# Kernel tuning notes

Measured on AMD Instinct MI355X. Metric: run time of the kernel, lower is better.

The kernel has to match this reference:

```python
import jax, jax.numpy as jnp
import numpy as np

S = 512            # sample_points along each ray
VD = VH = VW = 128  # voxel volume shape (drr.density.shape)
DET = 128           # detector H = W


def setup_inputs() -> dict:
    key = jax.random.key(0)
    k1, k2, k3 = jax.random.split(key, 3)
    B = 2
    pred_frontal = jax.random.uniform(k1, (B, 1, DET, DET), dtype=jnp.float32)
    pred_lateral = jax.random.uniform(k2, (B, 1, DET, DET), dtype=jnp.float32)
    ii, jj = jnp.meshgrid(jnp.arange(DET, dtype=jnp.float32),
                          jnp.arange(DET, dtype=jnp.float32), indexing='ij')
    # frontal: source behind volume on -z, detector plane at z=328
    source_F = jnp.array([[64.0, 64.0, -200.0]], dtype=jnp.float32)
    target_F = jnp.stack([ii, jj, jnp.full_like(ii, 328.0)], axis=-1)[None]  # (1,H,W,3)
    # lateral: source on -x, detector plane at x=328
    source_L = jnp.array([[-200.0, 64.0, 64.0]], dtype=jnp.float32)
    target_L = jnp.stack([jnp.full_like(ii, 328.0), ii, jj], axis=-1)[None]
    vol_gt_3d = jax.random.uniform(k3, (VD, VH, VW), dtype=jnp.float32)
    A_inv = jnp.eye(3, dtype=jnp.float32)   # drr.affine_inverse linear part
    t_inv = jnp.zeros(3, dtype=jnp.float32)  # drr.affine_inverse translation
    return {"pred_frontal": pred_frontal, "pred_lateral": pred_lateral,
            "source_F": source_F, "target_F": target_F,
            "source_L": source_L, "target_L": target_L,
            "vol_gt_3d": vol_gt_3d, "A_inv": A_inv, "t_inv": t_inv}


def _backproject(mask_2d, src, target_grid, A_inv, t_inv, threshold=0.5):
    # mask_2d: (H,W); src: (3,); target_grid: (H,W,3)
    active = (mask_2d > threshold).reshape(-1)          # (P,) bool
    det_pixels = target_grid.reshape(-1, 3)             # (P,3)
    ray_dirs = det_pixels - src[None, :]                 # (P,3)
    ray_len = jnp.linalg.norm(ray_dirs, axis=1, keepdims=True)  # (P,1)
    ray_dirs = ray_dirs / (ray_len + 1e-8)
    t_vals = jnp.linspace(0.0, 1.0, S, dtype=mask_2d.dtype)[None, :, None]  # (1,S,1)
    t_samples = t_vals * (ray_len[:, None, :] * 2.5)     # (P,S,1)
    world_pts = src[None, None, :] + ray_dirs[:, None, :] * t_samples  # (P,S,3)
    voxel = jnp.round(world_pts @ A_inv.T + t_inv).astype(jnp.int32)   # (P,S,3)
    valid = (active[:, None]
             & (voxel[..., 0] >= 0) & (voxel[..., 0] < VD)
             & (voxel[..., 1] >= 0) & (voxel[..., 1] < VH)
             & (voxel[..., 2] >= 0) & (voxel[..., 2] < VW))
    vi = jnp.clip(voxel, 0, jnp.array([VD - 1, VH - 1, VW - 1], dtype=jnp.int32))
    vol = jnp.zeros((VD, VH, VW), dtype=mask_2d.dtype)
    # set-to-1 scatter: max with {0,1} values; invalid samples write 0 (no-op)
    vol = vol.at[vi[..., 0], vi[..., 1], vi[..., 2]].max(valid.astype(mask_2d.dtype))
    return vol


def reference(pred_frontal, pred_lateral, source_F, target_F,
              source_L, target_L, vol_gt_3d, A_inv, t_inv):
    src_F, tgt_F = source_F[0], target_F[0]
    src_L, tgt_L = source_L[0], target_L[0]
    B = pred_frontal.shape[0]
    total = jnp.zeros((), dtype=pred_frontal.dtype)
    for i in range(B):
        vol_F = _backproject(pred_frontal[i, 0], src_F, tgt_F, A_inv, t_inv)
        vol_L = _backproject(pred_lateral[i, 0], src_L, tgt_L, A_inv, t_inv)
        p = jax.nn.sigmoid(vol_F + vol_L)  # values in sigmoid({0,1,2})
        bce = -jnp.mean(vol_gt_3d * jnp.log(p) + (1.0 - vol_gt_3d) * jnp.log1p(-p))
        total = total + bce
    return total / B
```

## Files before the change

### kernel.cpp

```cpp
#include <hip/hip_runtime.h>

#define DETN 128
#define NPIX (DETN * DETN)
#define VDIM 128
#define NVOX (VDIM * VDIM * VDIM)
#define NWORDS (NVOX / 32)
#define NSAMP 512
#define SPLITK 4

__global__ __launch_bounds__(256) void bp_kernel(
    const float* __restrict__ predF, const float* __restrict__ predL,
    const float* __restrict__ srcF,  const float* __restrict__ srcL,
    const float* __restrict__ tgtF,  const float* __restrict__ tgtL,
    const float* __restrict__ Ainv,  const float* __restrict__ tinv,
    unsigned int* __restrict__ flags)
{
    const int p     = blockIdx.y;
    const int view  = p & 1;
    const int batch = p >> 1;
    const int ray   = blockIdx.x * blockDim.x + threadIdx.x;

    const float* mask = (view ? predL : predF) + batch * NPIX;
    if (!(mask[ray] > 0.5f)) return;

    const float* src = view ? srcL : srcF;
    const float* tgt = (view ? tgtL : tgtF) + ray * 3;

    const float sx = src[0], sy = src[1], sz = src[2];
    float dx = tgt[0] - sx, dy = tgt[1] - sy, dz = tgt[2] - sz;
    const float len = sqrtf(dx * dx + dy * dy + dz * dz);
    const float inv = 1.0f / (len + 1e-8f);
    dx *= inv; dy *= inv; dz *= inv;

    const float a00 = Ainv[0], a01 = Ainv[1], a02 = Ainv[2];
    const float a10 = Ainv[3], a11 = Ainv[4], a12 = Ainv[5];
    const float a20 = Ainv[6], a21 = Ainv[7], a22 = Ainv[8];
    const float qcx = a00 * sx + a01 * sy + a02 * sz + tinv[0];
    const float qcy = a10 * sx + a11 * sy + a12 * sz + tinv[1];
    const float qcz = a20 * sx + a21 * sy + a22 * sz + tinv[2];
    const float qdx = a00 * dx + a01 * dy + a02 * dz;
    const float qdy = a10 * dx + a11 * dy + a12 * dz;
    const float qdz = a20 * dx + a21 * dy + a22 * dz;

    const float tmax = len * 2.5f;
    const float dt   = tmax * (1.0f / 511.0f);

    float tlo = 0.0f, thi = tmax;
    {
        const float c[3] = {qcx, qcy, qcz};
        const float d[3] = {qdx, qdy, qdz};
        #pragma unroll
        for (int j = 0; j < 3; ++j) {
            if (fabsf(d[j]) < 1e-8f) {
                if (c[j] < -0.6f || c[j] > 127.6f) thi = -1.0f;
            } else {
                const float ta = (-0.6f  - c[j]) / d[j];
                const float tb = (127.6f - c[j]) / d[j];
                tlo = fmaxf(tlo, fminf(ta, tb));
                thi = fminf(thi, fmaxf(ta, tb));
            }
        }
    }
    if (tlo > thi) return;
    const int klo = max(0, (int)ceilf(tlo / dt));
    const int khi = min(NSAMP - 1, (int)floorf(thi / dt));

    const int n   = khi - klo + 1;
    const int per = (n + SPLITK - 1) / SPLITK;
    const int k0  = klo + (int)blockIdx.z * per;
    const int k1  = min(khi, k0 + per - 1);
    if (k0 > khi) return;

    unsigned int* __restrict__ vol = flags + (size_t)p * NWORDS;
    int      curw = -1;
    unsigned bits = 0;
    for (int k = k0; k <= k1; ++k) {
        const float t  = (float)k * dt;
        const float qx = fmaf(qdx, t, qcx);
        const float qy = fmaf(qdy, t, qcy);
        const float qz = fmaf(qdz, t, qcz);
        const int ix = (int)rintf(qx);
        const int iy = (int)rintf(qy);
        const int iz = (int)rintf(qz);
        if ((unsigned)ix < (unsigned)VDIM && (unsigned)iy < (unsigned)VDIM &&
            (unsigned)iz < (unsigned)VDIM) {
            const int maj = view ? iz : ix;
            const int pk  = view ? ix : iz;
            const int w   = (maj << 9) | (iy << 2) | (pk >> 5);
            const unsigned bit = 1u << (pk & 31);
            if (w == curw) {
                bits |= bit;
            } else {
                if (curw >= 0) atomicOr(&vol[curw], bits);
                curw = w; bits = bit;
            }
        }
    }
    if (curw >= 0) atomicOr(&vol[curw], bits);
}

__global__ __launch_bounds__(256) void transpose_kernel(
    const unsigned int* __restrict__ flags,
    unsigned int* __restrict__ latz, int B)
{
    const int idx = blockIdx.x * blockDim.x + threadIdx.x;
    const int b = idx >> 16;
    const int w = idx & (NWORDS - 1);
    if (b >= B) return;
    const int x = w >> 9;
    const int y = (w >> 2) & 127;
    const int Z = w & 3;
    const unsigned int* __restrict__ src = flags + (size_t)(2 * b + 1) * NWORDS;
    const int base = (y << 2) | (x >> 5);
    const int sh   = x & 31;
    unsigned out = 0;
    #pragma unroll
    for (int zz = 0; zz < 32; ++zz) {
        const unsigned m = src[(((Z << 5) + zz) << 9) | base];
        out |= ((m >> sh) & 1u) << zz;
    }
    latz[(size_t)b * NWORDS + w] = out;
}

__global__ __launch_bounds__(256) void loss_kernel(
    const unsigned int* __restrict__ flags,
    const unsigned int* __restrict__ latz,
    const float* __restrict__ gt,
    float* __restrict__ out, int B, float scale)
{
    const int w = blockIdx.x * blockDim.x + threadIdx.x;
    float acc = 0.0f;
    if (w < NWORDS) {
        const float4* __restrict__ g4 = (const float4*)(gt + (size_t)w * 32);
        float g[32];
        #pragma unroll
        for (int q = 0; q < 8; ++q) {
            const float4 v = g4[q];
            g[4 * q + 0] = v.x; g[4 * q + 1] = v.y;
            g[4 * q + 2] = v.z; g[4 * q + 3] = v.w;
        }
        for (int b = 0; b < B; ++b) {
            const unsigned F = flags[(size_t)(2 * b) * NWORDS + w];
            const unsigned L = latz[(size_t)b * NWORDS + w];
            const int n2 = __popc(F & L);
            const int n1 = __popc(F | L) - n2;
            const int n0 = 32 - n1 - n2;
            acc += 0.6931471806f * (float)n0 + 1.3132616875f * (float)n1 +
                   2.1269280110f * (float)n2;
            float s = 0.0f;
            #pragma unroll
            for (int i = 0; i < 32; ++i) {
                s += g[i] * (float)(((F >> i) & 1u) + ((L >> i) & 1u));
            }
            acc -= s;
        }
    }

    #pragma unroll
    for (int off = 32; off > 0; off >>= 1) acc += __shfl_down(acc, off);

    __shared__ float smem[4];
    const int wid  = threadIdx.x >> 6;
    const int lane = threadIdx.x & 63;
    if (lane == 0) smem[wid] = acc;
    __syncthreads();
    if (threadIdx.x == 0) {
        const float tot = smem[0] + smem[1] + smem[2] + smem[3];
        atomicAdd(out, tot * scale);
    }
}

extern "C" void kernel_launch(void* const* d_in, const int* in_sizes, int n_in,
                              void* d_out, int out_size, void* d_ws, size_t ws_size,
                              hipStream_t stream) {
    const float* predF = (const float*)d_in[0];
    const float* predL = (const float*)d_in[1];
    const float* srcF  = (const float*)d_in[2];
    const float* tgtF  = (const float*)d_in[3];
    const float* srcL  = (const float*)d_in[4];
    const float* tgtL  = (const float*)d_in[5];
    const float* gt    = (const float*)d_in[6];
    const float* Ainv  = (const float*)d_in[7];
    const float* tinv  = (const float*)d_in[8];

    const int B = in_sizes[0] / NPIX;
    unsigned int* flags = (unsigned int*)d_ws;
    unsigned int* latz  = flags + (size_t)(2 * B) * NWORDS;

    hipMemsetAsync(flags, 0, (size_t)(2 * B) * NWORDS * sizeof(unsigned int), stream);
    hipMemsetAsync(d_out, 0, sizeof(float), stream);

    dim3 gridBp(NPIX / 256, 2 * B, SPLITK);
    bp_kernel<<<gridBp, 256, 0, stream>>>(predF, predL, srcF, srcL,
                                          tgtF, tgtL, Ainv, tinv, flags);

    transpose_kernel<<<(B * NWORDS) / 256, 256, 0, stream>>>(flags, latz, B);

    const float scale = 1.0f / ((float)NVOX * (float)B);
    loss_kernel<<<NWORDS / 256, 256, 0, stream>>>(flags, latz, gt,
                                                  (float*)d_out, B, scale);
}
```

Measured before the change: 114.8 us.

## Fuse memset, backprojection, transpose and loss into one cooperative kernel

Replaces two memsets and three kernel launches with a single cooperative kernel of 256 blocks. The kernel clears the bit volumes, runs the ray backprojection as a grid-stride loop, and computes the loss, with grid-wide syncs between the phases. The lateral transpose is folded into the loss phase, so the intermediate latz buffer and its write/read round trip go away. In exchange, the ray work now runs on a fixed 256-block grid instead of a large launch, and grid.sync adds barrier cost; the loss phase also does 32 strided gathers per word directly.

Measured after the change: 180.0 us. +56.7%, slower.

```diff
diff --git a/kernel.cpp b/kernel.cpp
--- a/kernel.cpp
+++ b/kernel.cpp
@@ -1,4 +1,7 @@
 #include <hip/hip_runtime.h>
+#include <hip/hip_cooperative_groups.h>
+
+namespace cg = cooperative_groups;
 
 #define DETN 128
 #define NPIX (DETN * DETN)
@@ -7,18 +10,19 @@
 #define NWORDS (NVOX / 32)
 #define NSAMP 512
 #define SPLITK 4
-
-__global__ __launch_bounds__(256) void bp_kernel(
+#define NBLK 256
+#define NTHR (NBLK * 256)
+
+__device__ __forceinline__ void do_ray(
+    int p, int ray, int seg,
     const float* __restrict__ predF, const float* __restrict__ predL,
     const float* __restrict__ srcF,  const float* __restrict__ srcL,
     const float* __restrict__ tgtF,  const float* __restrict__ tgtL,
     const float* __restrict__ Ainv,  const float* __restrict__ tinv,
     unsigned int* __restrict__ flags)
 {
-    const int p     = blockIdx.y;
     const int view  = p & 1;
     const int batch = p >> 1;
-    const int ray   = blockIdx.x * blockDim.x + threadIdx.x;
 
     const float* mask = (view ? predL : predF) + batch * NPIX;
     if (!(mask[ray] > 0.5f)) return;
@@ -67,7 +71,7 @@
 
     const int n   = khi - klo + 1;
     const int per = (n + SPLITK - 1) / SPLITK;
-    const int k0  = klo + (int)blockIdx.z * per;
+    const int k0  = klo + seg * per;
     const int k1  = min(khi, k0 + per - 1);
     if (k0 > khi) return;
 
@@ -99,38 +103,49 @@
     if (curw >= 0) atomicOr(&vol[curw], bits);
 }
 
-__global__ __launch_bounds__(256) void transpose_kernel(
-    const unsigned int* __restrict__ flags,
-    unsigned int* __restrict__ latz, int B)
+__global__ __launch_bounds__(256) void fused_kernel(
+    const float* __restrict__ predF, const float* __restrict__ predL,
+    const float* __restrict__ srcF,  const float* __restrict__ srcL,
+    const float* __restrict__ tgtF,  const float* __restrict__ tgtL,
+    const float* __restrict__ gt,
+    const float* __restrict__ Ainv,  const float* __restrict__ tinv,
+    unsigned int* __restrict__ flags, float* __restrict__ out,
+    int B, float scale)
 {
-    const int idx = blockIdx.x * blockDim.x + threadIdx.x;
-    const int b = idx >> 16;
-    const int w = idx & (NWORDS - 1);
-    if (b >= B) return;
-    const int x = w >> 9;
-    const int y = (w >> 2) & 127;
-    const int Z = w & 3;
-    const unsigned int* __restrict__ src = flags + (size_t)(2 * b + 1) * NWORDS;
-    const int base = (y << 2) | (x >> 5);
-    const int sh   = x & 31;
-    unsigned out = 0;
-    #pragma unroll
-    for (int zz = 0; zz < 32; ++zz) {
-        const unsigned m = src[(((Z << 5) + zz) << 9) | base];
-        out |= ((m >> sh) & 1u) << zz;
-    }
-    latz[(size_t)b * NWORDS + w] = out;
-}
-
-__global__ __launch_bounds__(256) void loss_kernel(
-    const unsigned int* __restrict__ flags,
-    const unsigned int* __restrict__ latz,
-    const float* __restrict__ gt,
-    float* __restrict__ out, int B, float scale)
-{
-    const int w = blockIdx.x * blockDim.x + threadIdx.x;
+    cg::grid_group grid = cg::this_grid();
+    const int tid = blockIdx.x * blockDim.x + threadIdx.x;
+
+    {
+        const int total4 = (2 * B * NWORDS) >> 2;
+        uint4* f4 = (uint4*)flags;
+        const uint4 z = make_uint4(0u, 0u, 0u, 0u);
+        for (int i = tid; i < total4; i += NTHR) f4[i] = z;
+        if (tid == 0) *out = 0.0f;
+    }
+    grid.sync();
+
+    {
+        const int ntask = 2 * B * NPIX * SPLITK;
+        for (int t = tid; t < ntask; t += NTHR) {
+            const int ray  = t & (NPIX - 1);
+            const int rest = t >> 14;
+            const int p    = rest % (2 * B);
+            const int seg  = rest / (2 * B);
+            do_ray(p, ray, seg, predF, predL, srcF, srcL, tgtF, tgtL,
+                   Ainv, tinv, flags);
+        }
+    }
+    grid.sync();
+
     float acc = 0.0f;
-    if (w < NWORDS) {
+    {
+        const int w = tid;
+        const int x = w >> 9;
+        const int y = (w >> 2) & 127;
+        const int Z = w & 3;
+        const int base = (y << 2) | (x >> 5);
+        const int sh   = x & 31;
+
         const float4* __restrict__ g4 = (const float4*)(gt + (size_t)w * 32);
         float g[32];
         #pragma unroll
@@ -139,9 +154,16 @@
             g[4 * q + 0] = v.x; g[4 * q + 1] = v.y;
             g[4 * q + 2] = v.z; g[4 * q + 3] = v.w;
         }
+
         for (int b = 0; b < B; ++b) {
             const unsigned F = flags[(size_t)(2 * b) * NWORDS + w];
-            const unsigned L = latz[(size_t)b * NWORDS + w];
+            const unsigned int* __restrict__ sl =
+                flags + (size_t)(2 * b + 1) * NWORDS;
+            unsigned L = 0;
+            #pragma unroll
+            for (int zz = 0; zz < 32; ++zz) {
+                L |= ((sl[(((Z << 5) + zz) << 9) | base] >> sh) & 1u) << zz;
+            }
             const int n2 = __popc(F & L);
             const int n1 = __popc(F | L) - n2;
             const int n0 = 32 - n1 - n2;
@@ -183,20 +205,16 @@
     const float* Ainv  = (const float*)d_in[7];
     const float* tinv  = (const float*)d_in[8];
 
-    const int B = in_sizes[0] / NPIX;
+    int B = in_sizes[0] / NPIX;
     unsigned int* flags = (unsigned int*)d_ws;
-    unsigned int* latz  = flags + (size_t)(2 * B) * NWORDS;
-
-    hipMemsetAsync(flags, 0, (size_t)(2 * B) * NWORDS * sizeof(unsigned int), stream);
-    hipMemsetAsync(d_out, 0, sizeof(float), stream);
-
-    dim3 gridBp(NPIX / 256, 2 * B, SPLITK);
-    bp_kernel<<<gridBp, 256, 0, stream>>>(predF, predL, srcF, srcL,
-                                          tgtF, tgtL, Ainv, tinv, flags);
-
-    transpose_kernel<<<(B * NWORDS) / 256, 256, 0, stream>>>(flags, latz, B);
-
-    const float scale = 1.0f / ((float)NVOX * (float)B);
-    loss_kernel<<<NWORDS / 256, 256, 0, stream>>>(flags, latz, gt,
-                                                  (float*)d_out, B, scale);
+    float* outp = (float*)d_out;
+    float scale = 1.0f / ((float)NVOX * (float)B);
+
+    void* args[] = {
+        (void*)&predF, (void*)&predL, (void*)&srcF, (void*)&srcL,
+        (void*)&tgtF,  (void*)&tgtL,  (void*)&gt,   (void*)&Ainv,
+        (void*)&tinv,  (void*)&flags, (void*)&outp, (void*)&B, (void*)&scale
+    };
+    hipLaunchCooperativeKernel((void*)fused_kernel, dim3(NBLK), dim3(256),
+                               args, 0, stream);
 }
```

## Fuse lateral bit transpose into loss kernel and drop output memset

Applied to the files above, without the earlier changes.

Removes the separate transpose kernel and its intermediate buffer by gathering the lateral-view bits directly inside the loss kernel, with each word split across four threads (8 bits each) to raise parallelism. The output zeroing memset is replaced by a single-thread store in the backprojection kernel. This saves a launch, a memset and a global round trip, but the loss kernel now does strided gathers from the lateral flags, and more threads take part in the reduction atomics.

Result: slower. 119.9 us (+4.4%).

```diff
diff --git a/kernel.cpp b/kernel.cpp
--- a/kernel.cpp
+++ b/kernel.cpp
@@ -13,8 +13,13 @@
     const float* __restrict__ srcF,  const float* __restrict__ srcL,
     const float* __restrict__ tgtF,  const float* __restrict__ tgtL,
     const float* __restrict__ Ainv,  const float* __restrict__ tinv,
-    unsigned int* __restrict__ flags)
+    unsigned int* __restrict__ flags, float* __restrict__ out)
 {
+    if (blockIdx.x == 0 && blockIdx.y == 0 && blockIdx.z == 0 &&
+        threadIdx.x == 0) {
+        *out = 0.0f;
+    }
+
     const int p     = blockIdx.y;
     const int view  = p & 1;
     const int batch = p >> 1;
@@ -99,61 +104,52 @@
     if (curw >= 0) atomicOr(&vol[curw], bits);
 }
 
-__global__ __launch_bounds__(256) void transpose_kernel(
+__global__ __launch_bounds__(256) void loss_kernel(
     const unsigned int* __restrict__ flags,
-    unsigned int* __restrict__ latz, int B)
+    const float* __restrict__ gt,
+    float* __restrict__ out, int B, float scale)
 {
-    const int idx = blockIdx.x * blockDim.x + threadIdx.x;
-    const int b = idx >> 16;
-    const int w = idx & (NWORDS - 1);
-    if (b >= B) return;
+    const int tid = blockIdx.x * blockDim.x + threadIdx.x;
+    const int w   = tid >> 2;
+    const int sub = tid & 3;
     const int x = w >> 9;
     const int y = (w >> 2) & 127;
     const int Z = w & 3;
-    const unsigned int* __restrict__ src = flags + (size_t)(2 * b + 1) * NWORDS;
     const int base = (y << 2) | (x >> 5);
     const int sh   = x & 31;
-    unsigned out = 0;
-    #pragma unroll
-    for (int zz = 0; zz < 32; ++zz) {
-        const unsigned m = src[(((Z << 5) + zz) << 9) | base];
-        out |= ((m >> sh) & 1u) << zz;
+    const int zoff = (Z << 5) + (sub << 3);
+
+    const float4* __restrict__ g4 =
+        (const float4*)(gt + (size_t)w * 32 + (size_t)sub * 8);
+    float g[8];
+    {
+        const float4 v0 = g4[0], v1 = g4[1];
+        g[0] = v0.x; g[1] = v0.y; g[2] = v0.z; g[3] = v0.w;
+        g[4] = v1.x; g[5] = v1.y; g[6] = v1.z; g[7] = v1.w;
     }
-    latz[(size_t)b * NWORDS + w] = out;
-}
 
-__global__ __launch_bounds__(256) void loss_kernel(
-    const unsigned int* __restrict__ flags,
-    const unsigned int* __restrict__ latz,
-    const float* __restrict__ gt,
-    float* __restrict__ out, int B, float scale)
-{
-    const int w = blockIdx.x * blockDim.x + threadIdx.x;
     float acc = 0.0f;
-    if (w < NWORDS) {
-        const float4* __restrict__ g4 = (const float4*)(gt + (size_t)w * 32);
-        float g[32];
+    for (int b = 0; b < B; ++b) {
+        const unsigned Fw = flags[(size_t)(2 * b) * NWORDS + w];
+        const unsigned Fb = (Fw >> (sub << 3)) & 0xffu;
+        const unsigned int* __restrict__ sl =
+            flags + (size_t)(2 * b + 1) * NWORDS;
+        unsigned Lb = 0;
         #pragma unroll
-        for (int q = 0; q < 8; ++q) {
-            const float4 v = g4[q];
-            g[4 * q + 0] = v.x; g[4 * q + 1] = v.y;
-            g[4 * q + 2] = v.z; g[4 * q + 3] = v.w;
+        for (int jj = 0; jj < 8; ++jj) {
+            Lb |= ((sl[((zoff + jj) << 9) | base] >> sh) & 1u) << jj;
         }
-        for (int b = 0; b < B; ++b) {
-            const unsigned F = flags[(size_t)(2 * b) * NWORDS + w];
-            const unsigned L = latz[(size_t)b * NWORDS + w];
-            const int n2 = __popc(F & L);
-            const int n1 = __popc(F | L) - n2;
-            const int n0 = 32 - n1 - n2;
-            acc += 0.6931471806f * (float)n0 + 1.3132616875f * (float)n1 +
-                   2.1269280110f * (float)n2;
-            float s = 0.0f;
-            #pragma unroll
-            for (int i = 0; i < 32; ++i) {
-                s += g[i] * (float)(((F >> i) & 1u) + ((L >> i) & 1u));
-            }
-            acc -= s;
+        const int n2 = __popc(Fb & Lb);
+        const int n1 = __popc(Fb | Lb) - n2;
+        const int n0 = 8 - n1 - n2;
+        acc += 0.6931471806f * (float)n0 + 1.3132616875f * (float)n1 +
+               2.1269280110f * (float)n2;
+        float s = 0.0f;
+        #pragma unroll
+        for (int i = 0; i < 8; ++i) {
+            s += g[i] * (float)(((Fb >> i) & 1u) + ((Lb >> i) & 1u));
         }
+        acc -= s;
     }
 
     #pragma unroll
@@ -185,18 +181,14 @@
 
     const int B = in_sizes[0] / NPIX;
     unsigned int* flags = (unsigned int*)d_ws;
-    unsigned int* latz  = flags + (size_t)(2 * B) * NWORDS;
+    float* outp = (float*)d_out;
 
     hipMemsetAsync(flags, 0, (size_t)(2 * B) * NWORDS * sizeof(unsigned int), stream);
-    hipMemsetAsync(d_out, 0, sizeof(float), stream);
 
     dim3 gridBp(NPIX / 256, 2 * B, SPLITK);
     bp_kernel<<<gridBp, 256, 0, stream>>>(predF, predL, srcF, srcL,
-                                          tgtF, tgtL, Ainv, tinv, flags);
-
-    transpose_kernel<<<(B * NWORDS) / 256, 256, 0, stream>>>(flags, latz, B);
+                                          tgtF, tgtL, Ainv, tinv, flags, outp);
 
     const float scale = 1.0f / ((float)NVOX * (float)B);
-    loss_kernel<<<NWORDS / 256, 256, 0, stream>>>(flags, latz, gt,
-                                                  (float*)d_out, B, scale);
+    loss_kernel<<<(4 * NWORDS) / 256, 256, 0, stream>>>(flags, gt, outp, B, scale);
 }
```

## Fuse lateral bit-transpose into loss kernel via shared memory; drop output memset

Applied to the files above, without the earlier changes.

Removes the separate transpose kernel and its intermediate buffer. Each loss block now stages the needed lateral and frontal flag words in LDS and rebuilds the transposed lateral bits on the fly. The output zeroing moves into the backprojection kernel, which saves one memset launch. The loss kernel now hardcodes B=2 and retiles its words so that one block covers a 32x2x4 word tile.

After: 109.9 us. -4.3%, faster.

```diff
diff --git a/kernel.cpp b/kernel.cpp
--- a/kernel.cpp
+++ b/kernel.cpp
@@ -13,8 +13,13 @@
     const float* __restrict__ srcF,  const float* __restrict__ srcL,
     const float* __restrict__ tgtF,  const float* __restrict__ tgtL,
     const float* __restrict__ Ainv,  const float* __restrict__ tinv,
-    unsigned int* __restrict__ flags)
+    unsigned int* __restrict__ flags, float* __restrict__ out)
 {
+    if (blockIdx.x == 0 && blockIdx.y == 0 && blockIdx.z == 0 &&
+        threadIdx.x == 0) {
+        *out = 0.0f;
+    }
+
     const int p     = blockIdx.y;
     const int view  = p & 1;
     const int batch = p >> 1;
@@ -99,72 +104,84 @@
     if (curw >= 0) atomicOr(&vol[curw], bits);
 }
 
-__global__ __launch_bounds__(256) void transpose_kernel(
-    const unsigned int* __restrict__ flags,
-    unsigned int* __restrict__ latz, int B)
-{
-    const int idx = blockIdx.x * blockDim.x + threadIdx.x;
-    const int b = idx >> 16;
-    const int w = idx & (NWORDS - 1);
-    if (b >= B) return;
-    const int x = w >> 9;
-    const int y = (w >> 2) & 127;
-    const int Z = w & 3;
-    const unsigned int* __restrict__ src = flags + (size_t)(2 * b + 1) * NWORDS;
-    const int base = (y << 2) | (x >> 5);
-    const int sh   = x & 31;
-    unsigned out = 0;
-    #pragma unroll
-    for (int zz = 0; zz < 32; ++zz) {
-        const unsigned m = src[(((Z << 5) + zz) << 9) | base];
-        out |= ((m >> sh) & 1u) << zz;
-    }
-    latz[(size_t)b * NWORDS + w] = out;
-}
-
 __global__ __launch_bounds__(256) void loss_kernel(
     const unsigned int* __restrict__ flags,
-    const unsigned int* __restrict__ latz,
     const float* __restrict__ gt,
-    float* __restrict__ out, int B, float scale)
+    float* __restrict__ out, float scale)
 {
-    const int w = blockIdx.x * blockDim.x + threadIdx.x;
+    __shared__ unsigned latw[2][2][128];
+    __shared__ unsigned fst[2][256];
+    __shared__ float    smem[4];
+
+    const int X0 = blockIdx.x & 3;
+    const int y0 = (blockIdx.x >> 2) << 1;
+    const int tid = threadIdx.x;
+
+    #pragma unroll
+    for (int b = 0; b < 2; ++b) {
+        {
+            const int r  = tid;
+            const int yi = r >> 7;
+            const int z  = r & 127;
+            latw[b][yi][z] =
+                flags[(size_t)(2 * b + 1) * NWORDS + (z << 9) + ((y0 + yi) << 2) + X0];
+        }
+        {
+            const int r  = tid;
+            const int xi = r >> 3;
+            const int yi = (r >> 2) & 1;
+            const int Zi = r & 3;
+            fst[b][r] =
+                flags[(size_t)(2 * b) * NWORDS + ((32 * X0 + xi) << 9) +
+                      ((y0 + yi) << 2) + Zi];
+        }
+    }
+    __syncthreads();
+
+    const int xi = tid & 31;
+    const int yi = (tid >> 5) & 1;
+    const int Zi = tid >> 6;
+    const int w  = ((32 * X0 + xi) << 9) | ((y0 + yi) << 2) | Zi;
+
+    const float4* __restrict__ g4 = (const float4*)(gt + (size_t)w * 32);
+    float g[32];
+    #pragma unroll
+    for (int q = 0; q < 8; ++q) {
+        const float4 v = g4[q];
+        g[4 * q + 0] = v.x; g[4 * q + 1] = v.y;
+        g[4 * q + 2] = v.z; g[4 * q + 3] = v.w;
+    }
+
     float acc = 0.0f;
-    if (w < NWORDS) {
-        const float4* __restrict__ g4 = (const float4*)(gt + (size_t)w * 32);
-        float g[32];
+    #pragma unroll
+    for (int b = 0; b < 2; ++b) {
+        const unsigned F = fst[b][(xi << 3) | (yi << 2) | Zi];
+        unsigned L = 0;
         #pragma unroll
-        for (int q = 0; q < 8; ++q) {
-            const float4 v = g4[q];
-            g[4 * q + 0] = v.x; g[4 * q + 1] = v.y;
-            g[4 * q + 2] = v.z; g[4 * q + 3] = v.w;
-        }
-        for (int b = 0; b < B; ++b) {
-            const unsigned F = flags[(size_t)(2 * b) * NWORDS + w];
-            const unsigned L = latz[(size_t)b * NWORDS + w];
-            const int n2 = __popc(F & L);
-            const int n1 = __popc(F | L) - n2;
-            const int n0 = 32 - n1 - n2;
-            acc += 0.6931471806f * (float)n0 + 1.3132616875f * (float)n1 +
-                   2.1269280110f * (float)n2;
-            float s = 0.0f;
-            #pragma unroll
-            for (int i = 0; i < 32; ++i) {
-                s += g[i] * (float)(((F >> i) & 1u) + ((L >> i) & 1u));
-            }
-            acc -= s;
-        }
+        for (int zz = 0; zz < 32; ++zz) {
+            L |= ((latw[b][yi][(Zi << 5) + zz] >> xi) & 1u) << zz;
+        }
+        const int n2 = __popc(F & L);
+        const int n1 = __popc(F | L) - n2;
+        const int n0 = 32 - n1 - n2;
+        acc += 0.6931471806f * (float)n0 + 1.3132616875f * (float)n1 +
+               2.1269280110f * (float)n2;
+        float s = 0.0f;
+        #pragma unroll
+        for (int i = 0; i < 32; ++i) {
+            s += g[i] * (float)(((F >> i) & 1u) + ((L >> i) & 1u));
+        }
+        acc -= s;
     }
 
     #pragma unroll
     for (int off = 32; off > 0; off >>= 1) acc += __shfl_down(acc, off);
 
-    __shared__ float smem[4];
-    const int wid  = threadIdx.x >> 6;
-    const int lane = threadIdx.x & 63;
+    const int wid  = tid >> 6;
+    const int lane = tid & 63;
     if (lane == 0) smem[wid] = acc;
     __syncthreads();
-    if (threadIdx.x == 0) {
+    if (tid == 0) {
         const float tot = smem[0] + smem[1] + smem[2] + smem[3];
         atomicAdd(out, tot * scale);
     }
@@ -185,18 +202,14 @@
 
     const int B = in_sizes[0] / NPIX;
     unsigned int* flags = (unsigned int*)d_ws;
-    unsigned int* latz  = flags + (size_t)(2 * B) * NWORDS;
+    float* outp = (float*)d_out;
 
     hipMemsetAsync(flags, 0, (size_t)(2 * B) * NWORDS * sizeof(unsigned int), stream);
-    hipMemsetAsync(d_out, 0, sizeof(float), stream);
 
     dim3 gridBp(NPIX / 256, 2 * B, SPLITK);
     bp_kernel<<<gridBp, 256, 0, stream>>>(predF, predL, srcF, srcL,
-                                          tgtF, tgtL, Ainv, tinv, flags);
-
-    transpose_kernel<<<(B * NWORDS) / 256, 256, 0, stream>>>(flags, latz, B);
+                                          tgtF, tgtL, Ainv, tinv, flags, outp);
 
     const float scale = 1.0f / ((float)NVOX * (float)B);
-    loss_kernel<<<NWORDS / 256, 256, 0, stream>>>(flags, latz, gt,
-                                                  (float*)d_out, B, scale);
+    loss_kernel<<<256, 256, 0, stream>>>(flags, gt, outp, scale);
 }
```
